# Performance work log

Hardware: AMD Instinct MI355X
Metric: run time of the kernel (lower is better)

Reference implementation:

```python
import jax, jax.numpy as jnp
import numpy as np

N_NODES = 100000
N_EDGES = 1600000
DIN = 128
DOUT = 128
N_SUP = 2


def setup_inputs() -> dict:
    key = jax.random.key(0)
    k = jax.random.split(key, 6)
    x = jax.random.normal(k[0], (N_NODES, DIN), dtype=jnp.float32)
    w = jax.random.normal(k[1], (N_SUP, DIN, DOUT), dtype=jnp.float32) * (1.0 / np.sqrt(DIN))
    bias = jax.random.normal(k[2], (DOUT,), dtype=jnp.float32) * 0.01
    sup_vals = jax.random.uniform(k[3], (N_SUP, N_EDGES), dtype=jnp.float32)
    sup_rows = jax.random.randint(k[4], (N_SUP, N_EDGES), 0, N_NODES, dtype=jnp.int32)
    sup_cols = jax.random.randint(k[5], (N_SUP, N_EDGES), 0, N_NODES, dtype=jnp.int32)
    return {"x": x, "w": w, "bias": bias, "sup_vals": sup_vals,
            "sup_rows": sup_rows, "sup_cols": sup_cols}


def _spmm(vals, rows, cols, dense):
    # COO sparse [N,N] @ dense [N,D] -> [N,D]
    gathered = vals[:, None] * dense[cols]        # [E, D]
    return jax.ops.segment_sum(gathered, rows, num_segments=N_NODES)


def reference(x, w, bias, sup_vals, sup_rows, sup_cols):
    # pre_sup_i = x @ w_i for each support: [S, N, Dout]
    pre = jnp.einsum('nd,sdo->sno', x, w)
    # SpMM per support, vmapped over the support axis, then summed
    supports = jax.vmap(_spmm)(sup_vals, sup_rows, sup_cols, pre)  # [S, N, Dout]
    out = supports.sum(axis=0) + bias
    return jax.nn.relu(out)
```

## Files before the change

kernel.cpp:

```cpp
#include <hip/hip_runtime.h>

#define N_NODES 100000
#define N_EDGES 1600000
#define DIN 128
#define DOUT 128
#define N_SUP 2
#define E_TOT (N_SUP * N_EDGES)

#define BIN_ROWS 128
#define BSHIFT 7
#define NBINS ((N_NODES + BIN_ROWS - 1) / BIN_ROWS)
#define CAP 4608

#define SC_EPT 16
#define SC_BLOCK 256
#define SC_CHUNK (SC_EPT * SC_BLOCK)
#define NBLK_SC ((E_TOT + SC_CHUNK - 1) / SC_CHUNK)

#define GEMM_ROWS 128
#define LDK 136

typedef float        f32x2 __attribute__((ext_vector_type(2)));
typedef float        f32x4 __attribute__((ext_vector_type(4)));
typedef unsigned int u32;
typedef u32          u32x2 __attribute__((ext_vector_type(2)));
typedef u32          u32x4 __attribute__((ext_vector_type(4)));
typedef short        bf16x8 __attribute__((ext_vector_type(8)));

static __device__ __forceinline__ u32 pack_bf16x2(float lo, float hi) {
    u32 ul = __float_as_uint(lo);
    u32 uh = __float_as_uint(hi);
    ul = (ul + 0x7FFFu + ((ul >> 16) & 1u)) >> 16;
    uh = ((uh + 0x7FFFu + ((uh >> 16) & 1u)) >> 16) << 16;
    return ul | uh;
}

__global__ __launch_bounds__(256) void wconv_kernel(const float* __restrict__ w,
                                                    u32* __restrict__ wTb) {
    const int s = blockIdx.x;
    const int n = threadIdx.x >> 1;
    const int kh = (threadIdx.x & 1) * 64;
    const float* wp = w + (size_t)s * DIN * DOUT + n;
    u32 o[32];
    #pragma unroll
    for (int j = 0; j < 32; j++) {
        const float lo = wp[(size_t)(kh + 2 * j) * DOUT];
        const float hi = wp[(size_t)(kh + 2 * j + 1) * DOUT];
        o[j] = pack_bf16x2(lo, hi);
    }
    u32* op = wTb + ((size_t)s * 128 + n) * 64 + kh / 2;
    #pragma unroll
    for (int j = 0; j < 8; j++)
        *(u32x4*)(op + j * 4) = *(u32x4*)&o[j * 4];
}

__global__ __launch_bounds__(256) void mfma_gemm_kernel(const float* __restrict__ x,
                                                        const u32* __restrict__ wTb,
                                                        u32* __restrict__ pre) {
    __shared__ alignas(16) unsigned short stage[2][GEMM_ROWS][LDK];
    float (*epi)[129] = (float (*)[129])(void*)stage;

    const int s = blockIdx.y;
    const int row0 = blockIdx.x * GEMM_ROWS;
    const int t = threadIdx.x;
    const int lane = t & 63;
    const int wv = t >> 6;

    {
        const int r = t >> 1;
        const int half = t & 1;
        const int gr = row0 + r;
        u32* dst = (u32*)&stage[0][r][half * 64];
        u32 o[32];
        if (gr < N_NODES) {
            const float* p = x + (size_t)gr * DIN + half * 64;
            #pragma unroll
            for (int j = 0; j < 16; j++) {
                const f32x4 a = *(const f32x4*)(p + j * 4);
                o[2 * j]     = pack_bf16x2(a.x, a.y);
                o[2 * j + 1] = pack_bf16x2(a.z, a.w);
            }
        } else {
            #pragma unroll
            for (int j = 0; j < 32; j++) o[j] = 0;
        }
        #pragma unroll
        for (int j = 0; j < 8; j++)
            *(u32x4*)(dst + j * 4) = *(u32x4*)&o[j * 4];
        const u32* wp = wTb + ((size_t)s * 128 + r) * 64 + half * 32;
        u32* wdst = (u32*)&stage[1][r][half * 64];
        #pragma unroll
        for (int j = 0; j < 8; j++)
            *(u32x4*)(wdst + j * 4) = *(const u32x4*)(wp + j * 4);
    }
    __syncthreads();

    const int q = lane >> 4;
    const int ml = lane & 15;
    const int m0 = wv * 32;

    f32x4 acc[2][8];
    #pragma unroll
    for (int mt = 0; mt < 2; mt++)
        #pragma unroll
        for (int nt = 0; nt < 8; nt++) acc[mt][nt] = (f32x4){0.f, 0.f, 0.f, 0.f};

    #pragma unroll
    for (int kt = 0; kt < 4; kt++) {
        const int k0 = kt * 32 + q * 8;
        const bf16x8 a0 = *(const bf16x8*)&stage[0][m0 + ml][k0];
        const bf16x8 a1 = *(const bf16x8*)&stage[0][m0 + 16 + ml][k0];
        #pragma unroll
        for (int nt = 0; nt < 8; nt++) {
            const bf16x8 b = *(const bf16x8*)&stage[1][nt * 16 + ml][k0];
            acc[0][nt] = __builtin_amdgcn_mfma_f32_16x16x32_bf16(a0, b, acc[0][nt], 0, 0, 0);
            acc[1][nt] = __builtin_amdgcn_mfma_f32_16x16x32_bf16(a1, b, acc[1][nt], 0, 0, 0);
        }
    }
    __syncthreads();

    #pragma unroll
    for (int mt = 0; mt < 2; mt++)
        #pragma unroll
        for (int nt = 0; nt < 8; nt++)
            #pragma unroll
            for (int r = 0; r < 4; r++)
                epi[m0 + mt * 16 + q * 4 + r][nt * 16 + ml] = acc[mt][nt][r];
    __syncthreads();

    {
        const int row = t >> 1;
        const int half = t & 1;
        const int gr = row0 + row;
        if (gr < N_NODES) {
            u32 ov[32];
            #pragma unroll
            for (int j = 0; j < 32; j++)
                ov[j] = pack_bf16x2(epi[row][half * 64 + 2 * j],
                                    epi[row][half * 64 + 2 * j + 1]);
            u32* op = pre + ((size_t)s * N_NODES + gr) * 64 + half * 32;
            #pragma unroll
            for (int j = 0; j < 8; j++)
                __builtin_nontemporal_store(*(u32x4*)&ov[j * 4], (u32x4*)(op + j * 4));
        }
    }
}

__global__ __launch_bounds__(256) void initcur_kernel(int* __restrict__ bin_cursor) {
    const int b = blockIdx.x * 256 + threadIdx.x;
    if (b < NBINS) bin_cursor[b] = b * CAP;
}

__global__ __launch_bounds__(256) void binscatter_kernel(const int* __restrict__ rows,
                                                         const int* __restrict__ cols,
                                                         const float* __restrict__ vals,
                                                         int* __restrict__ bin_cursor,
                                                         u32x2* __restrict__ edata) {
    __shared__ int lcnt[NBINS];
    __shared__ int lbase[NBINS];
    const int t = threadIdx.x;
    for (int i = t; i < NBINS; i += 256) lcnt[i] = 0;
    __syncthreads();

    const int base = blockIdx.x * SC_CHUNK;
    int bin[SC_EPT], lpos[SC_EPT];
    u32x2 pay[SC_EPT];
    #pragma unroll
    for (int j = 0; j < SC_EPT; j++) {
        const int i = base + j * 256 + t;
        if (i < E_TOT) {
            const int r = __builtin_nontemporal_load(rows + i);
            const int c = __builtin_nontemporal_load(cols + i);
            const float v = __builtin_nontemporal_load(vals + i);
            const int b = r >> BSHIFT;
            bin[j] = b;
            lpos[j] = atomicAdd(&lcnt[b], 1);
            pay[j].x = (u32)(c + ((i >= N_EDGES) ? N_NODES : 0)) |
                       ((u32)(r & (BIN_ROWS - 1)) << 18);
            pay[j].y = __float_as_uint(v);
        } else {
            bin[j] = -1;
        }
    }
    __syncthreads();
    for (int b = t; b < NBINS; b += 256) {
        const int c = lcnt[b];
        if (c) lbase[b] = atomicAdd(&bin_cursor[b], c);
    }
    __syncthreads();
    #pragma unroll
    for (int j = 0; j < SC_EPT; j++) {
        if (bin[j] >= 0) edata[lbase[bin[j]] + lpos[j]] = pay[j];
    }
}

__global__ __launch_bounds__(256) void binsort_kernel(u32x2* __restrict__ edata,
                                                      const int* __restrict__ bin_cursor,
                                                      int2* __restrict__ rbe) {
    __shared__ u32x2 ebuf[CAP];
    __shared__ int rcnt[BIN_ROWS];
    __shared__ int rscan[BIN_ROWS];
    const int t = threadIdx.x;
    const int b = blockIdx.x;
    const int beg = b * CAP;
    const int cnt = min(bin_cursor[b] - beg, CAP);

    for (int e = t; e < cnt; e += 256)
        ebuf[e] = __builtin_nontemporal_load(edata + beg + e);
    if (t < BIN_ROWS) rcnt[t] = 0;
    __syncthreads();

    for (int e = t; e < cnt; e += 256)
        atomicAdd(&rcnt[ebuf[e].x >> 18], 1);
    __syncthreads();

    const int v = (t < BIN_ROWS) ? rcnt[t] : 0;
    if (t < BIN_ROWS) rscan[t] = v;
    __syncthreads();
    #pragma unroll
    for (int off = 1; off < BIN_ROWS; off <<= 1) {
        const int u = (t < BIN_ROWS && t >= off) ? rscan[t - off] : 0;
        __syncthreads();
        if (t < BIN_ROWS) rscan[t] += u;
        __syncthreads();
    }
    if (t < BIN_ROWS) {
        const int ex = rscan[t] - v;
        rcnt[t] = ex;
        const int row = b * BIN_ROWS + t;
        if (row < N_NODES) {
            int2 be;
            be.x = beg + ex;
            be.y = beg + ex + v;
            rbe[row] = be;
        }
    }
    __syncthreads();
    for (int e = t; e < cnt; e += 256) {
        const u32x2 d = ebuf[e];
        const int pos = beg + atomicAdd(&rcnt[d.x >> 18], 1);
        u32x2 o;
        o.x = d.x & 0x3FFFFu;
        o.y = d.y;
        edata[pos] = o;
    }
}

__global__ __launch_bounds__(256, 6) void gather_kernel(const u32* __restrict__ pre,
                                                        const u32x2* __restrict__ edata,
                                                        const int2* __restrict__ rbe,
                                                        const float* __restrict__ bias,
                                                        float* __restrict__ out) {
    const int lane = threadIdx.x & 63;
    const int wid = threadIdx.x >> 6;
    const int row = blockIdx.x * 4 + wid;
    if (row >= N_NODES) return;

    const int2 be = rbe[row];
    int e = be.x;
    const int end = be.y;

    float ax = 0.f, ay = 0.f;

    if (e + 8 <= end) {
        u32x2 d[8];
        #pragma unroll
        for (int j = 0; j < 8; j++)
            d[j] = __builtin_nontemporal_load(edata + e + j);
        for (;;) {
            u32 u[8];
            #pragma unroll
            for (int j = 0; j < 8; j++)
                u[j] = pre[(u32)((d[j].x << 6) + (u32)lane)];
            const int en = e + 8;
            const bool more = (en + 8 <= end);
            u32x2 dn[8];
            if (more) {
                #pragma unroll
                for (int j = 0; j < 8; j++)
                    dn[j] = __builtin_nontemporal_load(edata + en + j);
            }
            #pragma unroll
            for (int j = 0; j < 8; j++) {
                const float v = __uint_as_float(d[j].y);
                ax = fmaf(v, __uint_as_float(u[j] << 16), ax);
                ay = fmaf(v, __uint_as_float(u[j] & 0xFFFF0000u), ay);
            }
            e = en;
            if (!more) break;
            #pragma unroll
            for (int j = 0; j < 8; j++) d[j] = dn[j];
        }
    }
    for (; e + 4 <= end; e += 4) {
        u32x2 d[4];
        #pragma unroll
        for (int j = 0; j < 4; j++)
            d[j] = __builtin_nontemporal_load(edata + e + j);
        u32 u[4];
        #pragma unroll
        for (int j = 0; j < 4; j++)
            u[j] = pre[(u32)((d[j].x << 6) + (u32)lane)];
        #pragma unroll
        for (int j = 0; j < 4; j++) {
            const float v = __uint_as_float(d[j].y);
            ax = fmaf(v, __uint_as_float(u[j] << 16), ax);
            ay = fmaf(v, __uint_as_float(u[j] & 0xFFFF0000u), ay);
        }
    }
    for (; e < end; e++) {
        const u32x2 d = __builtin_nontemporal_load(edata + e);
        const u32 u = pre[(u32)((d.x << 6) + (u32)lane)];
        const float v = __uint_as_float(d.y);
        ax = fmaf(v, __uint_as_float(u << 16), ax);
        ay = fmaf(v, __uint_as_float(u & 0xFFFF0000u), ay);
    }

    const float2 b = *(const float2*)(bias + lane * 2);
    f32x2 r;
    r.x = fmaxf(ax + b.x, 0.f);
    r.y = fmaxf(ay + b.y, 0.f);
    __builtin_nontemporal_store(r, (f32x2*)(out + (size_t)row * DOUT + lane * 2));
}

extern "C" void kernel_launch(void* const* d_in, const int* in_sizes, int n_in,
                              void* d_out, int out_size, void* d_ws, size_t ws_size,
                              hipStream_t stream) {
    (void)in_sizes; (void)n_in; (void)out_size; (void)ws_size;
    const float* x        = (const float*)d_in[0];
    const float* w        = (const float*)d_in[1];
    const float* bias     = (const float*)d_in[2];
    const float* sup_vals = (const float*)d_in[3];
    const int*   sup_rows = (const int*)d_in[4];
    const int*   sup_cols = (const int*)d_in[5];
    float* out = (float*)d_out;

    char* ws = (char*)d_ws;
    u32*   pre       = (u32*)ws;
    u32x2* edata     = (u32x2*)(ws + (size_t)N_SUP * N_NODES * 64 * 4);
    int2*  rbe       = (int2*)((char*)edata + (size_t)NBINS * CAP * 8);
    int*   bin_cursor= (int*)(rbe + N_NODES);
    u32*   wTb       = (u32*)(bin_cursor + NBINS + 2);

    wconv_kernel<<<N_SUP, 256, 0, stream>>>(w, wTb);
    {
        dim3 grid((N_NODES + GEMM_ROWS - 1) / GEMM_ROWS, N_SUP);
        mfma_gemm_kernel<<<grid, 256, 0, stream>>>(x, wTb, pre);
    }
    initcur_kernel<<<(NBINS + 255) / 256, 256, 0, stream>>>(bin_cursor);
    binscatter_kernel<<<NBLK_SC, 256, 0, stream>>>(sup_rows, sup_cols, sup_vals,
                                                   bin_cursor, edata);
    binsort_kernel<<<NBINS, 256, 0, stream>>>(edata, bin_cursor, rbe);
    gather_kernel<<<(N_NODES + 3) / 4, 256, 0, stream>>>(pre, edata, rbe, bias, out);
}
```

Measured before the change: 391.7 us.

## Split gather wavefront into four edge groups with 16-byte row loads

The gather kernel now divides each 64-lane wavefront into four 16-lane subgroups. Each subgroup processes a different edge and loads a full 256-byte bf16 row with 16-byte loads, and the partial sums are combined with cross-lane shuffles at the end. This aims to raise memory-level parallelism and cut the number of load instructions, at the cost of extra shuffle work and 8 accumulators per lane. The binsort kernel now keeps each edge's local position from the counting pass, so the second atomic pass goes away, but this adds register pressure. The cursor-init kernel is also folded into the weight-conversion launch to save one launch.

```diff
diff --git a/kernel.cpp b/kernel.cpp
--- a/kernel.cpp
+++ b/kernel.cpp
@@ -11,6 +11,7 @@
 #define BSHIFT 7
 #define NBINS ((N_NODES + BIN_ROWS - 1) / BIN_ROWS)
 #define CAP 4608
+#define EPT_BS 18
 
 #define SC_EPT 16
 #define SC_BLOCK 256
@@ -35,8 +36,14 @@
     return ul | uh;
 }
 
-__global__ __launch_bounds__(256) void wconv_kernel(const float* __restrict__ w,
-                                                    u32* __restrict__ wTb) {
+__global__ __launch_bounds__(256) void wconv_init_kernel(const float* __restrict__ w,
+                                                         u32* __restrict__ wTb,
+                                                         int* __restrict__ bin_cursor) {
+    if (blockIdx.x >= N_SUP) {
+        const int b = (blockIdx.x - N_SUP) * 256 + threadIdx.x;
+        if (b < NBINS) bin_cursor[b] = b * CAP;
+        return;
+    }
     const int s = blockIdx.x;
     const int n = threadIdx.x >> 1;
     const int kh = (threadIdx.x & 1) * 64;
@@ -144,11 +151,6 @@
                 __builtin_nontemporal_store(*(u32x4*)&ov[j * 4], (u32x4*)(op + j * 4));
         }
     }
-}
-
-__global__ __launch_bounds__(256) void initcur_kernel(int* __restrict__ bin_cursor) {
-    const int b = blockIdx.x * 256 + threadIdx.x;
-    if (b < NBINS) bin_cursor[b] = b * CAP;
 }
 
 __global__ __launch_bounds__(256) void binscatter_kernel(const int* __restrict__ rows,
@@ -199,7 +201,7 @@
                                                       int2* __restrict__ rbe) {
     __shared__ u32x2 ebuf[CAP];
     __shared__ int rcnt[BIN_ROWS];
-    __shared__ int rscan[BIN_ROWS];
+    __shared__ int rbase[BIN_ROWS];
     const int t = threadIdx.x;
     const int b = blockIdx.x;
     const int beg = b * CAP;
@@ -210,23 +212,27 @@
     if (t < BIN_ROWS) rcnt[t] = 0;
     __syncthreads();
 
-    for (int e = t; e < cnt; e += 256)
-        atomicAdd(&rcnt[ebuf[e].x >> 18], 1);
+    int lp[EPT_BS];
+    #pragma unroll
+    for (int k = 0; k < EPT_BS; k++) {
+        const int e = t + k * 256;
+        if (e < cnt) lp[k] = atomicAdd(&rcnt[ebuf[e].x >> 18], 1);
+    }
     __syncthreads();
 
     const int v = (t < BIN_ROWS) ? rcnt[t] : 0;
-    if (t < BIN_ROWS) rscan[t] = v;
+    if (t < BIN_ROWS) rbase[t] = v;
     __syncthreads();
     #pragma unroll
     for (int off = 1; off < BIN_ROWS; off <<= 1) {
-        const int u = (t < BIN_ROWS && t >= off) ? rscan[t - off] : 0;
+        const int u = (t < BIN_ROWS && t >= off) ? rbase[t - off] : 0;
         __syncthreads();
-        if (t < BIN_ROWS) rscan[t] += u;
+        if (t < BIN_ROWS) rbase[t] += u;
         __syncthreads();
     }
     if (t < BIN_ROWS) {
-        const int ex = rscan[t] - v;
-        rcnt[t] = ex;
+        const int ex = rbase[t] - v;
+        rbase[t] = ex;
         const int row = b * BIN_ROWS + t;
         if (row < N_NODES) {
             int2 be;
@@ -236,13 +242,17 @@
         }
     }
     __syncthreads();
-    for (int e = t; e < cnt; e += 256) {
-        const u32x2 d = ebuf[e];
-        const int pos = beg + atomicAdd(&rcnt[d.x >> 18], 1);
-        u32x2 o;
-        o.x = d.x & 0x3FFFFu;
-        o.y = d.y;
-        edata[pos] = o;
+    #pragma unroll
+    for (int k = 0; k < EPT_BS; k++) {
+        const int e = t + k * 256;
+        if (e < cnt) {
+            const u32x2 d = ebuf[e];
+            const int pos = beg + rbase[d.x >> 18] + lp[k];
+            u32x2 o;
+            o.x = d.x & 0x3FFFFu;
+            o.y = d.y;
+            edata[pos] = o;
+        }
     }
 }
 
@@ -252,6 +262,8 @@
                                                         const float* __restrict__ bias,
                                                         float* __restrict__ out) {
     const int lane = threadIdx.x & 63;
+    const int sub = lane >> 4;
+    const int fl = lane & 15;
     const int wid = threadIdx.x >> 6;
     const int row = blockIdx.x * 4 + wid;
     if (row >= N_NODES) return;
@@ -260,67 +272,77 @@
     int e = be.x;
     const int end = be.y;
 
-    float ax = 0.f, ay = 0.f;
-
-    if (e + 8 <= end) {
+    f32x4 a0 = (f32x4){0.f, 0.f, 0.f, 0.f};
+    f32x4 a1 = (f32x4){0.f, 0.f, 0.f, 0.f};
+
+    for (; e + 32 <= end; e += 32) {
         u32x2 d[8];
         #pragma unroll
         for (int j = 0; j < 8; j++)
-            d[j] = __builtin_nontemporal_load(edata + e + j);
-        for (;;) {
-            u32 u[8];
-            #pragma unroll
-            for (int j = 0; j < 8; j++)
-                u[j] = pre[(u32)((d[j].x << 6) + (u32)lane)];
-            const int en = e + 8;
-            const bool more = (en + 8 <= end);
-            u32x2 dn[8];
-            if (more) {
-                #pragma unroll
-                for (int j = 0; j < 8; j++)
-                    dn[j] = __builtin_nontemporal_load(edata + en + j);
+            d[j] = __builtin_nontemporal_load(edata + e + j * 4 + sub);
+        u32x4 u[8];
+        #pragma unroll
+        for (int j = 0; j < 8; j++)
+            u[j] = __builtin_nontemporal_load(
+                       (const u32x4*)(pre + ((size_t)d[j].x << 6) + fl * 4));
+        #pragma unroll
+        for (int j = 0; j < 8; j++) {
+            const float v = __uint_as_float(d[j].y);
+            #pragma unroll
+            for (int k = 0; k < 4; k++) {
+                a0[k] = fmaf(v, __uint_as_float(u[j][k] << 16), a0[k]);
+                a1[k] = fmaf(v, __uint_as_float(u[j][k] & 0xFFFF0000u), a1[k]);
             }
-            #pragma unroll
-            for (int j = 0; j < 8; j++) {
-                const float v = __uint_as_float(d[j].y);
-                ax = fmaf(v, __uint_as_float(u[j] << 16), ax);
-                ay = fmaf(v, __uint_as_float(u[j] & 0xFFFF0000u), ay);
-            }
-            e = en;
-            if (!more) break;
-            #pragma unroll
-            for (int j = 0; j < 8; j++) d[j] = dn[j];
         }
     }
     for (; e + 4 <= end; e += 4) {
-        u32x2 d[4];
-        #pragma unroll
-        for (int j = 0; j < 4; j++)
-            d[j] = __builtin_nontemporal_load(edata + e + j);
-        u32 u[4];
-        #pragma unroll
-        for (int j = 0; j < 4; j++)
-            u[j] = pre[(u32)((d[j].x << 6) + (u32)lane)];
-        #pragma unroll
-        for (int j = 0; j < 4; j++) {
-            const float v = __uint_as_float(d[j].y);
-            ax = fmaf(v, __uint_as_float(u[j] << 16), ax);
-            ay = fmaf(v, __uint_as_float(u[j] & 0xFFFF0000u), ay);
-        }
-    }
-    for (; e < end; e++) {
-        const u32x2 d = __builtin_nontemporal_load(edata + e);
-        const u32 u = pre[(u32)((d.x << 6) + (u32)lane)];
+        const u32x2 d = __builtin_nontemporal_load(edata + e + sub);
+        const u32x4 u = __builtin_nontemporal_load(
+                            (const u32x4*)(pre + ((size_t)d.x << 6) + fl * 4));
         const float v = __uint_as_float(d.y);
-        ax = fmaf(v, __uint_as_float(u << 16), ax);
-        ay = fmaf(v, __uint_as_float(u & 0xFFFF0000u), ay);
-    }
-
-    const float2 b = *(const float2*)(bias + lane * 2);
-    f32x2 r;
-    r.x = fmaxf(ax + b.x, 0.f);
-    r.y = fmaxf(ay + b.y, 0.f);
-    __builtin_nontemporal_store(r, (f32x2*)(out + (size_t)row * DOUT + lane * 2));
+        #pragma unroll
+        for (int k = 0; k < 4; k++) {
+            a0[k] = fmaf(v, __uint_as_float(u[k] << 16), a0[k]);
+            a1[k] = fmaf(v, __uint_as_float(u[k] & 0xFFFF0000u), a1[k]);
+        }
+    }
+    const int rem = end - e;
+    if (rem > 0) {
+        const int idx = (sub < rem) ? sub : 0;
+        const u32x2 d = __builtin_nontemporal_load(edata + e + idx);
+        const u32x4 u = __builtin_nontemporal_load(
+                            (const u32x4*)(pre + ((size_t)d.x << 6) + fl * 4));
+        const float v = (sub < rem) ? __uint_as_float(d.y) : 0.f;
+        #pragma unroll
+        for (int k = 0; k < 4; k++) {
+            a0[k] = fmaf(v, __uint_as_float(u[k] << 16), a0[k]);
+            a1[k] = fmaf(v, __uint_as_float(u[k] & 0xFFFF0000u), a1[k]);
+        }
+    }
+
+    #pragma unroll
+    for (int k = 0; k < 4; k++) {
+        a0[k] += __shfl_xor(a0[k], 16);
+        a0[k] += __shfl_xor(a0[k], 32);
+        a1[k] += __shfl_xor(a1[k], 16);
+        a1[k] += __shfl_xor(a1[k], 32);
+    }
+
+    if (sub == 0) {
+        const float* bp = bias + fl * 8;
+        float* op = out + (size_t)row * DOUT + fl * 8;
+        f32x4 r0, r1;
+        r0.x = fmaxf(a0[0] + bp[0], 0.f);
+        r0.y = fmaxf(a1[0] + bp[1], 0.f);
+        r0.z = fmaxf(a0[1] + bp[2], 0.f);
+        r0.w = fmaxf(a1[1] + bp[3], 0.f);
+        r1.x = fmaxf(a0[2] + bp[4], 0.f);
+        r1.y = fmaxf(a1[2] + bp[5], 0.f);
+        r1.z = fmaxf(a0[3] + bp[6], 0.f);
+        r1.w = fmaxf(a1[3] + bp[7], 0.f);
+        __builtin_nontemporal_store(r0, (f32x4*)op);
+        __builtin_nontemporal_store(r1, (f32x4*)(op + 4));
+    }
 }
 
 extern "C" void kernel_launch(void* const* d_in, const int* in_sizes, int n_in,
@@ -342,12 +364,11 @@
     int*   bin_cursor= (int*)(rbe + N_NODES);
     u32*   wTb       = (u32*)(bin_cursor + NBINS + 2);
 
-    wconv_kernel<<<N_SUP, 256, 0, stream>>>(w, wTb);
+    wconv_init_kernel<<<N_SUP + (NBINS + 255) / 256, 256, 0, stream>>>(w, wTb, bin_cursor);
     {
         dim3 grid((N_NODES + GEMM_ROWS - 1) / GEMM_ROWS, N_SUP);
         mfma_gemm_kernel<<<grid, 256, 0, stream>>>(x, wTb, pre);
     }
-    initcur_kernel<<<(NBINS + 255) / 256, 256, 0, stream>>>(bin_cursor);
     binscatter_kernel<<<NBLK_SC, 256, 0, stream>>>(sup_rows, sup_cols, sup_vals,
                                                    bin_cursor, edata);
     binsort_kernel<<<NBINS, 256, 0, stream>>>(edata, bin_cursor, rbe);
```

New measurement: 448.7 us. 1.15x slower.

## Fuse bin sort with gather in shared memory and merge cursor init into wconv

Applied to the files above, without the earlier changes.

Merges the per-bin counting sort and the row gather into one kernel. Edges stay in LDS and a shared index permutation replaces writing the sorted edge list and per-row ranges back to global memory. The cursor initialisation also moves into the weight-conversion kernel, removing a launch. In exchange, each 512-thread block holds about 46KB of LDS and handles 128 rows with only 8 waves, so occupancy and latency hiding for the random pre gathers may drop.

```diff
diff --git a/kernel.cpp b/kernel.cpp
--- a/kernel.cpp
+++ b/kernel.cpp
@@ -12,6 +12,9 @@
 #define NBINS ((N_NODES + BIN_ROWS - 1) / BIN_ROWS)
 #define CAP 4608
 
+#define SG_THREADS 512
+#define EPT_SG ((CAP + SG_THREADS - 1) / SG_THREADS)
+
 #define SC_EPT 16
 #define SC_BLOCK 256
 #define SC_CHUNK (SC_EPT * SC_BLOCK)
@@ -35,8 +38,14 @@
     return ul | uh;
 }
 
-__global__ __launch_bounds__(256) void wconv_kernel(const float* __restrict__ w,
-                                                    u32* __restrict__ wTb) {
+__global__ __launch_bounds__(256) void wconv_init_kernel(const float* __restrict__ w,
+                                                         u32* __restrict__ wTb,
+                                                         int* __restrict__ bin_cursor) {
+    if (blockIdx.x >= N_SUP) {
+        const int b = (blockIdx.x - N_SUP) * 256 + threadIdx.x;
+        if (b < NBINS) bin_cursor[b] = b * CAP;
+        return;
+    }
     const int s = blockIdx.x;
     const int n = threadIdx.x >> 1;
     const int kh = (threadIdx.x & 1) * 64;
@@ -144,11 +153,6 @@
                 __builtin_nontemporal_store(*(u32x4*)&ov[j * 4], (u32x4*)(op + j * 4));
         }
     }
-}
-
-__global__ __launch_bounds__(256) void initcur_kernel(int* __restrict__ bin_cursor) {
-    const int b = blockIdx.x * 256 + threadIdx.x;
-    if (b < NBINS) bin_cursor[b] = b * CAP;
 }
 
 __global__ __launch_bounds__(256) void binscatter_kernel(const int* __restrict__ rows,
@@ -194,133 +198,114 @@
     }
 }
 
-__global__ __launch_bounds__(256) void binsort_kernel(u32x2* __restrict__ edata,
-                                                      const int* __restrict__ bin_cursor,
-                                                      int2* __restrict__ rbe) {
+__global__ __launch_bounds__(SG_THREADS) void sortgather_kernel(
+        const u32* __restrict__ pre,
+        const u32x2* __restrict__ edata,
+        const int* __restrict__ bin_cursor,
+        const float* __restrict__ bias,
+        float* __restrict__ out) {
     __shared__ u32x2 ebuf[CAP];
+    __shared__ unsigned short pidx[CAP];
     __shared__ int rcnt[BIN_ROWS];
-    __shared__ int rscan[BIN_ROWS];
+    __shared__ int rbase[BIN_ROWS];
     const int t = threadIdx.x;
     const int b = blockIdx.x;
     const int beg = b * CAP;
     const int cnt = min(bin_cursor[b] - beg, CAP);
 
-    for (int e = t; e < cnt; e += 256)
+    for (int e = t; e < cnt; e += SG_THREADS)
         ebuf[e] = __builtin_nontemporal_load(edata + beg + e);
     if (t < BIN_ROWS) rcnt[t] = 0;
     __syncthreads();
 
-    for (int e = t; e < cnt; e += 256)
-        atomicAdd(&rcnt[ebuf[e].x >> 18], 1);
+    int lp[EPT_SG];
+    #pragma unroll
+    for (int k = 0; k < EPT_SG; k++) {
+        const int e = t + k * SG_THREADS;
+        if (e < cnt) lp[k] = atomicAdd(&rcnt[ebuf[e].x >> 18], 1);
+    }
     __syncthreads();
 
     const int v = (t < BIN_ROWS) ? rcnt[t] : 0;
-    if (t < BIN_ROWS) rscan[t] = v;
+    if (t < BIN_ROWS) rbase[t] = v;
     __syncthreads();
     #pragma unroll
     for (int off = 1; off < BIN_ROWS; off <<= 1) {
-        const int u = (t < BIN_ROWS && t >= off) ? rscan[t - off] : 0;
+        const int u = (t < BIN_ROWS && t >= off) ? rbase[t - off] : 0;
         __syncthreads();
-        if (t < BIN_ROWS) rscan[t] += u;
+        if (t < BIN_ROWS) rbase[t] += u;
         __syncthreads();
     }
-    if (t < BIN_ROWS) {
-        const int ex = rscan[t] - v;
-        rcnt[t] = ex;
-        const int row = b * BIN_ROWS + t;
-        if (row < N_NODES) {
-            int2 be;
-            be.x = beg + ex;
-            be.y = beg + ex + v;
-            rbe[row] = be;
-        }
-    }
-    __syncthreads();
-    for (int e = t; e < cnt; e += 256) {
-        const u32x2 d = ebuf[e];
-        const int pos = beg + atomicAdd(&rcnt[d.x >> 18], 1);
-        u32x2 o;
-        o.x = d.x & 0x3FFFFu;
-        o.y = d.y;
-        edata[pos] = o;
-    }
-}
-
-__global__ __launch_bounds__(256, 6) void gather_kernel(const u32* __restrict__ pre,
-                                                        const u32x2* __restrict__ edata,
-                                                        const int2* __restrict__ rbe,
-                                                        const float* __restrict__ bias,
-                                                        float* __restrict__ out) {
-    const int lane = threadIdx.x & 63;
-    const int wid = threadIdx.x >> 6;
-    const int row = blockIdx.x * 4 + wid;
-    if (row >= N_NODES) return;
-
-    const int2 be = rbe[row];
-    int e = be.x;
-    const int end = be.y;
-
-    float ax = 0.f, ay = 0.f;
-
-    if (e + 8 <= end) {
-        u32x2 d[8];
-        #pragma unroll
-        for (int j = 0; j < 8; j++)
-            d[j] = __builtin_nontemporal_load(edata + e + j);
-        for (;;) {
+    if (t < BIN_ROWS) rbase[t] -= v;
+    __syncthreads();
+
+    #pragma unroll
+    for (int k = 0; k < EPT_SG; k++) {
+        const int e = t + k * SG_THREADS;
+        if (e < cnt)
+            pidx[rbase[ebuf[e].x >> 18] + lp[k]] = (unsigned short)e;
+    }
+    __syncthreads();
+
+    const int lane = t & 63;
+    const int wid = t >> 6;
+    for (int rl = wid; rl < BIN_ROWS; rl += 8) {
+        const int row = b * BIN_ROWS + rl;
+        if (row >= N_NODES) continue;
+        int e = rbase[rl];
+        const int end = e + rcnt[rl];
+
+        float ax = 0.f, ay = 0.f;
+        for (; e + 8 <= end; e += 8) {
+            u32 col[8]; float val[8];
+            #pragma unroll
+            for (int j = 0; j < 8; j++) {
+                const u32x2 d = ebuf[pidx[e + j]];
+                col[j] = d.x & 0x3FFFFu;
+                val[j] = __uint_as_float(d.y);
+            }
             u32 u[8];
             #pragma unroll
             for (int j = 0; j < 8; j++)
-                u[j] = pre[(u32)((d[j].x << 6) + (u32)lane)];
-            const int en = e + 8;
-            const bool more = (en + 8 <= end);
-            u32x2 dn[8];
-            if (more) {
-                #pragma unroll
-                for (int j = 0; j < 8; j++)
-                    dn[j] = __builtin_nontemporal_load(edata + en + j);
-            }
+                u[j] = pre[(col[j] << 6) + (u32)lane];
             #pragma unroll
             for (int j = 0; j < 8; j++) {
-                const float v = __uint_as_float(d[j].y);
-                ax = fmaf(v, __uint_as_float(u[j] << 16), ax);
-                ay = fmaf(v, __uint_as_float(u[j] & 0xFFFF0000u), ay);
-            }
-            e = en;
-            if (!more) break;
-            #pragma unroll
-            for (int j = 0; j < 8; j++) d[j] = dn[j];
-        }
-    }
-    for (; e + 4 <= end; e += 4) {
-        u32x2 d[4];
-        #pragma unroll
-        for (int j = 0; j < 4; j++)
-            d[j] = __builtin_nontemporal_load(edata + e + j);
-        u32 u[4];
-        #pragma unroll
-        for (int j = 0; j < 4; j++)
-            u[j] = pre[(u32)((d[j].x << 6) + (u32)lane)];
-        #pragma unroll
-        for (int j = 0; j < 4; j++) {
-            const float v = __uint_as_float(d[j].y);
-            ax = fmaf(v, __uint_as_float(u[j] << 16), ax);
-            ay = fmaf(v, __uint_as_float(u[j] & 0xFFFF0000u), ay);
-        }
-    }
-    for (; e < end; e++) {
-        const u32x2 d = __builtin_nontemporal_load(edata + e);
-        const u32 u = pre[(u32)((d.x << 6) + (u32)lane)];
-        const float v = __uint_as_float(d.y);
-        ax = fmaf(v, __uint_as_float(u << 16), ax);
-        ay = fmaf(v, __uint_as_float(u & 0xFFFF0000u), ay);
-    }
-
-    const float2 b = *(const float2*)(bias + lane * 2);
-    f32x2 r;
-    r.x = fmaxf(ax + b.x, 0.f);
-    r.y = fmaxf(ay + b.y, 0.f);
-    __builtin_nontemporal_store(r, (f32x2*)(out + (size_t)row * DOUT + lane * 2));
+                ax = fmaf(val[j], __uint_as_float(u[j] << 16), ax);
+                ay = fmaf(val[j], __uint_as_float(u[j] & 0xFFFF0000u), ay);
+            }
+        }
+        for (; e + 4 <= end; e += 4) {
+            u32 col[4]; float val[4];
+            #pragma unroll
+            for (int j = 0; j < 4; j++) {
+                const u32x2 d = ebuf[pidx[e + j]];
+                col[j] = d.x & 0x3FFFFu;
+                val[j] = __uint_as_float(d.y);
+            }
+            u32 u[4];
+            #pragma unroll
+            for (int j = 0; j < 4; j++)
+                u[j] = pre[(col[j] << 6) + (u32)lane];
+            #pragma unroll
+            for (int j = 0; j < 4; j++) {
+                ax = fmaf(val[j], __uint_as_float(u[j] << 16), ax);
+                ay = fmaf(val[j], __uint_as_float(u[j] & 0xFFFF0000u), ay);
+            }
+        }
+        for (; e < end; e++) {
+            const u32x2 d = ebuf[pidx[e]];
+            const u32 u = pre[((d.x & 0x3FFFFu) << 6) + (u32)lane];
+            const float vv = __uint_as_float(d.y);
+            ax = fmaf(vv, __uint_as_float(u << 16), ax);
+            ay = fmaf(vv, __uint_as_float(u & 0xFFFF0000u), ay);
+        }
+
+        const float2 bb = *(const float2*)(bias + lane * 2);
+        f32x2 r;
+        r.x = fmaxf(ax + bb.x, 0.f);
+        r.y = fmaxf(ay + bb.y, 0.f);
+        __builtin_nontemporal_store(r, (f32x2*)(out + (size_t)row * DOUT + lane * 2));
+    }
 }
 
 extern "C" void kernel_launch(void* const* d_in, const int* in_sizes, int n_in,
@@ -338,18 +323,15 @@
     char* ws = (char*)d_ws;
     u32*   pre       = (u32*)ws;
     u32x2* edata     = (u32x2*)(ws + (size_t)N_SUP * N_NODES * 64 * 4);
-    int2*  rbe       = (int2*)((char*)edata + (size_t)NBINS * CAP * 8);
-    int*   bin_cursor= (int*)(rbe + N_NODES);
+    int*   bin_cursor= (int*)((char*)edata + (size_t)NBINS * CAP * 8);
     u32*   wTb       = (u32*)(bin_cursor + NBINS + 2);
 
-    wconv_kernel<<<N_SUP, 256, 0, stream>>>(w, wTb);
+    wconv_init_kernel<<<N_SUP + (NBINS + 255) / 256, 256, 0, stream>>>(w, wTb, bin_cursor);
     {
         dim3 grid((N_NODES + GEMM_ROWS - 1) / GEMM_ROWS, N_SUP);
         mfma_gemm_kernel<<<grid, 256, 0, stream>>>(x, wTb, pre);
     }
-    initcur_kernel<<<(NBINS + 255) / 256, 256, 0, stream>>>(bin_cursor);
     binscatter_kernel<<<NBLK_SC, 256, 0, stream>>>(sup_rows, sup_cols, sup_vals,
                                                    bin_cursor, edata);
-    binsort_kernel<<<NBINS, 256, 0, stream>>>(edata, bin_cursor, rbe);
-    gather_kernel<<<(N_NODES + 3) / 4, 256, 0, stream>>>(pre, edata, rbe, bias, out);
-}
+    sortgather_kernel<<<NBINS, SG_THREADS, 0, stream>>>(pre, edata, bin_cursor, bias, out);
+}
```

Result: slower. 403.8 us (+3.1%).

## Horizontally fuse GEMM halves with edge binning and sorting kernels

Applied to the files above, without the earlier changes.

Merges the cursor init into the weight-conversion kernel. Splits the two-support GEMM so that support 0 runs interleaved (odd/even block ids) with the bin-scatter kernel and support 1 with the bin-sort kernel. The intent is to cut launch count and overlap the compute-bound GEMM with the memory- and atomic-bound binning passes. In exchange, every block now reserves the GEMM's roughly 68 KB shared buffer, which lowers occupancy for the scatter and sort blocks that previously needed far less LDS.

```diff
diff --git a/kernel.cpp b/kernel.cpp
--- a/kernel.cpp
+++ b/kernel.cpp
@@ -18,7 +18,9 @@
 #define NBLK_SC ((E_TOT + SC_CHUNK - 1) / SC_CHUNK)
 
 #define GEMM_ROWS 128
+#define NBLK_GEMM ((N_NODES + GEMM_ROWS - 1) / GEMM_ROWS)
 #define LDK 136
+#define SMEM_BYTES (2 * GEMM_ROWS * LDK * 2)
 
 typedef float        f32x2 __attribute__((ext_vector_type(2)));
 typedef float        f32x4 __attribute__((ext_vector_type(4)));
@@ -35,8 +37,14 @@
     return ul | uh;
 }
 
-__global__ __launch_bounds__(256) void wconv_kernel(const float* __restrict__ w,
-                                                    u32* __restrict__ wTb) {
+__global__ __launch_bounds__(256) void wconv_init_kernel(const float* __restrict__ w,
+                                                         u32* __restrict__ wTb,
+                                                         int* __restrict__ bin_cursor) {
+    if (blockIdx.x >= N_SUP) {
+        const int b = (blockIdx.x - N_SUP) * 256 + threadIdx.x;
+        if (b < NBINS) bin_cursor[b] = b * CAP;
+        return;
+    }
     const int s = blockIdx.x;
     const int n = threadIdx.x >> 1;
     const int kh = (threadIdx.x & 1) * 64;
@@ -54,14 +62,15 @@
         *(u32x4*)(op + j * 4) = *(u32x4*)&o[j * 4];
 }
 
-__global__ __launch_bounds__(256) void mfma_gemm_kernel(const float* __restrict__ x,
-                                                        const u32* __restrict__ wTb,
-                                                        u32* __restrict__ pre) {
-    __shared__ alignas(16) unsigned short stage[2][GEMM_ROWS][LDK];
-    float (*epi)[129] = (float (*)[129])(void*)stage;
-
-    const int s = blockIdx.y;
-    const int row0 = blockIdx.x * GEMM_ROWS;
+static __device__ __forceinline__ void gemm_body(char* smem, int bidx, int s,
+                                                 const float* __restrict__ x,
+                                                 const u32* __restrict__ wTb,
+                                                 u32* __restrict__ pre) {
+    typedef unsigned short (*stage_p)[GEMM_ROWS][LDK];
+    stage_p stage = (stage_p)smem;
+    float (*epi)[129] = (float (*)[129])smem;
+
+    const int row0 = bidx * GEMM_ROWS;
     const int t = threadIdx.x;
     const int lane = t & 63;
     const int wv = t >> 6;
@@ -146,23 +155,19 @@
     }
 }
 
-__global__ __launch_bounds__(256) void initcur_kernel(int* __restrict__ bin_cursor) {
-    const int b = blockIdx.x * 256 + threadIdx.x;
-    if (b < NBINS) bin_cursor[b] = b * CAP;
-}
-
-__global__ __launch_bounds__(256) void binscatter_kernel(const int* __restrict__ rows,
-                                                         const int* __restrict__ cols,
-                                                         const float* __restrict__ vals,
-                                                         int* __restrict__ bin_cursor,
-                                                         u32x2* __restrict__ edata) {
-    __shared__ int lcnt[NBINS];
-    __shared__ int lbase[NBINS];
+static __device__ __forceinline__ void scatter_body(char* smem, int bidx,
+                                                    const int* __restrict__ rows,
+                                                    const int* __restrict__ cols,
+                                                    const float* __restrict__ vals,
+                                                    int* __restrict__ bin_cursor,
+                                                    u32x2* __restrict__ edata) {
+    int* lcnt = (int*)smem;
+    int* lbase = lcnt + NBINS;
     const int t = threadIdx.x;
     for (int i = t; i < NBINS; i += 256) lcnt[i] = 0;
     __syncthreads();
 
-    const int base = blockIdx.x * SC_CHUNK;
+    const int base = bidx * SC_CHUNK;
     int bin[SC_EPT], lpos[SC_EPT];
     u32x2 pay[SC_EPT];
     #pragma unroll
@@ -194,14 +199,14 @@
     }
 }
 
-__global__ __launch_bounds__(256) void binsort_kernel(u32x2* __restrict__ edata,
-                                                      const int* __restrict__ bin_cursor,
-                                                      int2* __restrict__ rbe) {
-    __shared__ u32x2 ebuf[CAP];
-    __shared__ int rcnt[BIN_ROWS];
-    __shared__ int rscan[BIN_ROWS];
+static __device__ __forceinline__ void sort_body(char* smem, int b,
+                                                 u32x2* __restrict__ edata,
+                                                 const int* __restrict__ bin_cursor,
+                                                 int2* __restrict__ rbe) {
+    u32x2* ebuf = (u32x2*)smem;
+    int* rcnt = (int*)(smem + CAP * 8);
+    int* rscan = rcnt + BIN_ROWS;
     const int t = threadIdx.x;
-    const int b = blockIdx.x;
     const int beg = b * CAP;
     const int cnt = min(bin_cursor[b] - beg, CAP);
 
@@ -244,6 +249,32 @@
         o.y = d.y;
         edata[pos] = o;
     }
+}
+
+__global__ __launch_bounds__(256) void fusedA_kernel(const int* __restrict__ rows,
+                                                     const int* __restrict__ cols,
+                                                     const float* __restrict__ vals,
+                                                     int* __restrict__ bin_cursor,
+                                                     u32x2* __restrict__ edata,
+                                                     const float* __restrict__ x,
+                                                     const u32* __restrict__ wTb,
+                                                     u32* __restrict__ pre) {
+    __shared__ alignas(16) char smem[SMEM_BYTES];
+    const int bid = blockIdx.x;
+    if (bid & 1) gemm_body(smem, bid >> 1, 0, x, wTb, pre);
+    else         scatter_body(smem, bid >> 1, rows, cols, vals, bin_cursor, edata);
+}
+
+__global__ __launch_bounds__(256) void fusedB_kernel(u32x2* __restrict__ edata,
+                                                     const int* __restrict__ bin_cursor,
+                                                     int2* __restrict__ rbe,
+                                                     const float* __restrict__ x,
+                                                     const u32* __restrict__ wTb,
+                                                     u32* __restrict__ pre) {
+    __shared__ alignas(16) char smem[SMEM_BYTES];
+    const int bid = blockIdx.x;
+    if (bid & 1) gemm_body(smem, bid >> 1, 1, x, wTb, pre);
+    else         sort_body(smem, bid >> 1, edata, bin_cursor, rbe);
 }
 
 __global__ __launch_bounds__(256, 6) void gather_kernel(const u32* __restrict__ pre,
@@ -342,14 +373,9 @@
     int*   bin_cursor= (int*)(rbe + N_NODES);
     u32*   wTb       = (u32*)(bin_cursor + NBINS + 2);
 
-    wconv_kernel<<<N_SUP, 256, 0, stream>>>(w, wTb);
-    {
-        dim3 grid((N_NODES + GEMM_ROWS - 1) / GEMM_ROWS, N_SUP);
-        mfma_gemm_kernel<<<grid, 256, 0, stream>>>(x, wTb, pre);
-    }
-    initcur_kernel<<<(NBINS + 255) / 256, 256, 0, stream>>>(bin_cursor);
-    binscatter_kernel<<<NBLK_SC, 256, 0, stream>>>(sup_rows, sup_cols, sup_vals,
-                                                   bin_cursor, edata);
-    binsort_kernel<<<NBINS, 256, 0, stream>>>(edata, bin_cursor, rbe);
+    wconv_init_kernel<<<N_SUP + (NBINS + 255) / 256, 256, 0, stream>>>(w, wTb, bin_cursor);
+    fusedA_kernel<<<NBLK_SC + NBLK_GEMM, 256, 0, stream>>>(sup_rows, sup_cols, sup_vals,
+                                                           bin_cursor, edata, x, wTb, pre);
+    fusedB_kernel<<<NBINS + NBLK_GEMM, 256, 0, stream>>>(edata, bin_cursor, rbe, x, wTb, pre);
     gather_kernel<<<(N_NODES + 3) / 4, 256, 0, stream>>>(pre, edata, rbe, bias, out);
 }
```

Result: faster. 377.1 us (-3.7%).
